# Kernel optimization log

Hardware: AMD Instinct MI355X
Metric: run time of the kernel (lower is better)

## Reference

```python
import jax, jax.numpy as jnp
import numpy as np

KS = 3            # kernel_size
DILS = (1, 2, 4)  # dilation_list == padding_list
EPS = 1e-5        # BN eps


def _unfold3(x, d):
    # emulate F.unfold(kernel=3, dilation=d, padding=d, stride=1).view(b, c, 9, h, w)
    b, c, h, w = x.shape
    xp = jnp.pad(x, ((0, 0), (0, 0), (d, d), (d, d)))
    pats = [xp[:, :, i * d:i * d + h, j * d:j * d + w] for i in range(KS) for j in range(KS)]
    return jnp.stack(pats, axis=2)


def _conv1x1(x, w, b):
    return jnp.einsum('bchw,oc->bohw', x, w) + b[None, :, None, None]


def _bn_relu(x, g, be, m, v):
    s = g / jnp.sqrt(v + EPS)
    return jax.nn.relu(x * s[None, :, None, None] + (be - m * s)[None, :, None, None])


def _proj(x, w1, b1, g1, be1, m1, v1, w2, b2, g2, be2, m2, v2):
    h = _bn_relu(_conv1x1(x, w1, b1), g1, be1, m1, v1)
    return _bn_relu(_conv1x1(h, w2, b2), g2, be2, m2, v2)


def setup_inputs():
    key = jax.random.key(0)
    Cin, Ck, Cv, Cout = 512, 256, 256, 512
    B, H, W = 4, 64, 64
    ks = iter(jax.random.split(key, 48))

    def nrm(shape, s=0.02):
        return jax.random.normal(next(ks), shape, jnp.float32) * s

    def bn(c):
        return (jnp.ones((c,), jnp.float32) + nrm((c,), 0.1),  # gamma
                nrm((c,), 0.1),                                 # beta
                nrm((c,), 0.1),                                 # running mean
                jax.random.uniform(next(ks), (c,), jnp.float32, 0.5, 1.5))  # running var

    inp = {"x": jax.random.normal(next(ks), (B, Cin, H, W), jnp.float32)}
    for p in ("k", "q"):
        g1, be1, m1, v1 = bn(Ck)
        g2, be2, m2, v2 = bn(Ck)
        inp.update({
            p + "1_w": nrm((Ck, Cin)), p + "1_b": nrm((Ck,)),
            p + "1_g": g1, p + "1_be": be1, p + "1_m": m1, p + "1_v": v1,
            p + "2_w": nrm((Ck, Ck)), p + "2_b": nrm((Ck,)),
            p + "2_g": g2, p + "2_be": be2, p + "2_m": m2, p + "2_v": v2,
        })
    inp["v_w"] = nrm((Cv, Cin)); inp["v_b"] = nrm((Cv,))
    inp["w_w"] = nrm((Cout, Cv)); inp["w_b"] = nrm((Cout,))
    return inp


def reference(x,
              k1_w, k1_b, k1_g, k1_be, k1_m, k1_v,
              k2_w, k2_b, k2_g, k2_be, k2_m, k2_v,
              q1_w, q1_b, q1_g, q1_be, q1_m, q1_v,
              q2_w, q2_b, q2_g, q2_be, q2_m, q2_v,
              v_w, v_b, w_w, w_b):
    # scale == 1: MaxPool2d(1x1-equivalent) and final bilinear resize are identities.
    value = _conv1x1(x, v_w, v_b)                                  # (b,cv,h,w)
    keyf = _proj(x, k1_w, k1_b, k1_g, k1_be, k1_m, k1_v,
                 k2_w, k2_b, k2_g, k2_be, k2_m, k2_v)              # (b,ck,h,w)
    query = _proj(x, q1_w, q1_b, q1_g, q1_be, q1_m, q1_v,
                  q2_w, q2_b, q2_g, q2_be, q2_m, q2_v)             # (b,ck,h,w)
    uk = jnp.concatenate([_unfold3(keyf, d) for d in DILS], axis=2)   # (b,ck,27,h,w)
    uv = jnp.concatenate([_unfold3(value, d) for d in DILS], axis=2)  # (b,cv,27,h,w)
    sim = jnp.sum(uk * query[:, :, None], axis=1, keepdims=True)      # (b,1,27,h,w)
    sim = jax.nn.softmax(sim, axis=2)
    context = jnp.sum(sim * uv, axis=2)                               # (b,cv,h,w)
    return _conv1x1(context, w_w, w_b)
```

## Files before the change

### kernel.cpp

```cpp
#include <hip/hip_runtime.h>

#define HW   4096
#define Hh   64
#define Ww   64
#define NB   27
#define EPSBN 1e-5f

typedef _Float16 f16x8 __attribute__((ext_vector_type(8)));
typedef _Float16 f16x4 __attribute__((ext_vector_type(4)));
typedef _Float16 f16x2 __attribute__((ext_vector_type(2)));
typedef float    f32x4 __attribute__((ext_vector_type(4)));

__device__ __forceinline__ void gld_lds16(const void* g, void* l) {
    __builtin_amdgcn_global_load_lds(
        (const __attribute__((address_space(1))) unsigned int*)g,
        (__attribute__((address_space(3))) unsigned int*)l, 16, 0, 0);
}

__global__ __launch_bounds__(256)
void cvt_w_kernel(const float* s0, const float* s1, const float* s2,
                  const float* s3, const float* s4, const float* s5,
                  _Float16* d0, _Float16* d1, _Float16* d2,
                  _Float16* d3, _Float16* d4, _Float16* d5)
{
    const int j = blockIdx.y;
    const float* s = j==0?s0: j==1?s1: j==2?s2: j==3?s3: j==4?s4: s5;
    _Float16*  d = j==0?d0: j==1?d1: j==2?d2: j==3?d3: j==4?d4: d5;
    const int  n = (j==3 || j==4) ? 65536 : 131072;
    const int  i = (blockIdx.x * 256 + threadIdx.x) * 8;
    if (i < n) {
        f16x8 h;
        #pragma unroll
        for (int k = 0; k < 8; ++k) h[k] = (_Float16)s[i + k];
        *(f16x8*)(d + i) = h;
    }
}

__global__ __launch_bounds__(256)
void cvt_x_kernel(const float* __restrict__ x, _Float16* __restrict__ xT)
{
    const int tx = threadIdx.x;
    const int ty = threadIdx.y;
    const int p  = blockIdx.x * 64 + tx;
    const int c0 = blockIdx.y * 32 + ty * 8;
    const int b  = blockIdx.z;
    const float* xp = x + ((size_t)b * 512 + c0) * HW + p;
    f16x8 h;
    #pragma unroll
    for (int i = 0; i < 8; ++i) h[i] = (_Float16)xp[(size_t)i * HW];
    *(f16x8*)(xT + ((size_t)b * HW + p) * 512 + c0) = h;
}

struct GJob {
    const _Float16* in;
    const _Float16* w;
    const float* b; const float* g; const float* be; const float* m; const float* v;
    _Float16* oh;
    float*    of;
};

__global__ __launch_bounds__(256)
void gemm128(GJob J0, GJob J1, GJob J2, int nmb0, int nmb01,
             int K, int JO, int mode)
{
    __shared__ _Float16 As[128 * 64];
    __shared__ _Float16 Bs[128 * 64];

    const int tid  = threadIdx.x;
    const int lane = tid & 63;
    const int w    = tid >> 6;
    const int lr   = lane & 15;
    const int lg   = lane >> 4;
    const int wm   = w & 1;
    const int wn   = w >> 1;

    const int bx = blockIdx.x;
    const int nb = (bx & 7) * 16 + (bx >> 3);
    const int mb = blockIdx.y;

    const bool i0 = mb < nmb0;
    const bool i1 = !i0 && mb < nmb01;
#define SELJ(f) (i0 ? J0.f : (i1 ? J1.f : J2.f))
    const _Float16* Jin = SELJ(in);
    const _Float16* Jw  = SELJ(w);
    const float* Jb  = SELJ(b);
    const float* Jg  = SELJ(g);
    const float* Jbe = SELJ(be);
    const float* Jm  = SELJ(m);
    const float* Jv  = SELJ(v);
    _Float16* Joh = SELJ(oh);
    float*    Jof = SELJ(of);
#undef SELJ
    const int obase = (mb - (i0 ? 0 : (i1 ? nmb0 : nmb01))) * 128;

    const int rowS = w * 32 + (lane >> 3);
    const int scol = (((lane & 7) ^ (lane >> 3)) << 3);
    const _Float16* aSrc = Jw  + (size_t)(obase + rowS) * K + scol;
    const _Float16* bSrc = Jin + (size_t)(nb * 128 + rowS) * K + scol;
    char* aDst = (char*)As + w * 4096;
    char* bDst = (char*)Bs + w * 4096;

    f32x4 acc[4][4] = {};

    const int nr = K >> 6;
    for (int rd = 0; rd < nr; ++rd) {
        __syncthreads();
        const int kb = rd * 64;
        #pragma unroll
        for (int j = 0; j < 4; ++j)
            gld_lds16(aSrc + (size_t)j * 8 * K + kb, aDst + j * 1024);
        #pragma unroll
        for (int j = 0; j < 4; ++j)
            gld_lds16(bSrc + (size_t)j * 8 * K + kb, bDst + j * 1024);
        __syncthreads();

        #pragma unroll
        for (int ks = 0; ks < 2; ++ks) {
            const int colx = (ks * 64 + lg * 16) ^ ((lr & 7) << 4);
            f16x8 afr[4], bfr[4];
            #pragma unroll
            for (int t = 0; t < 4; ++t) {
                afr[t] = *(const f16x8*)((const char*)As + (wm * 64 + t * 16 + lr) * 128 + colx);
                bfr[t] = *(const f16x8*)((const char*)Bs + (wn * 64 + t * 16 + lr) * 128 + colx);
            }
            #pragma unroll
            for (int ai = 0; ai < 4; ++ai)
                #pragma unroll
                for (int bj = 0; bj < 4; ++bj)
                    acc[ai][bj] = __builtin_amdgcn_mfma_f32_16x16x32_f16(
                        afr[ai], bfr[bj], acc[ai][bj], 0, 0, 0);
        }
    }

    const int relu = (Jg != nullptr);
    #pragma unroll
    for (int ai = 0; ai < 4; ++ai) {
        const int o4 = obase + wm * 64 + ai * 16 + lg * 4;
        float sc[4], of_[4];
        #pragma unroll
        for (int r = 0; r < 4; ++r) {
            const int o = o4 + r;
            if (Jg) { float s = Jg[o] * rsqrtf(Jv[o] + EPSBN); sc[r] = s; of_[r] = fmaf(Jb[o] - Jm[o], s, Jbe[o]); }
            else    { sc[r] = 1.f; of_[r] = Jb[o]; }
        }
        #pragma unroll
        for (int bj = 0; bj < 4; ++bj) {
            const int pg = nb * 128 + wn * 64 + bj * 16 + lr;
            float vv[4];
            #pragma unroll
            for (int r = 0; r < 4; ++r) {
                float t = fmaf(acc[ai][bj][r], sc[r], of_[r]);
                vv[r] = relu ? fmaxf(t, 0.f) : t;
            }
            if (mode == 0) {
                f16x4 h;
                #pragma unroll
                for (int r = 0; r < 4; ++r) h[r] = (_Float16)vv[r];
                *(f16x4*)(Joh + (size_t)pg * JO + o4) = h;
            } else {
                #pragma unroll
                for (int r = 0; r < 4; ++r)
                    Jof[((size_t)(pg >> 12) * JO + o4 + r) * HW + (pg & 4095)] = vv[r];
            }
        }
    }
}

__global__ __launch_bounds__(256)
void attn_fused(const _Float16* __restrict__ keyT, const _Float16* __restrict__ qryT,
                const _Float16* __restrict__ valT, _Float16* __restrict__ ctxT)
{
    const int tid  = threadIdx.x;
    const int slot = tid & 31;
    const int b    = blockIdx.y;
    const int p    = blockIdx.x * 8 + (tid >> 5);
    const int y    = p >> 6;
    const int xc   = p & 63;

    int   idx[NB];
    float valf[NB];
    #pragma unroll
    for (int n = 0; n < NB; ++n) {
        const int d  = (n < 9) ? 1 : (n < 18 ? 2 : 4);
        const int i  = (n / 3) % 3 - 1;
        const int j  = n % 3 - 1;
        const int yy = y + i * d, xx = xc + j * d;
        const bool ok = ((unsigned)yy < (unsigned)Hh) && ((unsigned)xx < (unsigned)Ww);
        idx[n]  = min(max(yy, 0), Hh - 1) * Ww + min(max(xx, 0), Ww - 1);
        valf[n] = ok ? 1.f : 0.f;
    }

    const size_t base = (size_t)b * HW * 256 + slot * 8;
    const f16x8 q8 = *(const f16x8*)(qryT + base + (size_t)p * 256);

    f16x2 qp[4];
    #pragma unroll
    for (int i = 0; i < 4; ++i)
        qp[i] = __builtin_shufflevector(q8, q8, 0, 1);
    qp[0] = __builtin_shufflevector(q8, q8, 0, 1);
    qp[1] = __builtin_shufflevector(q8, q8, 2, 3);
    qp[2] = __builtin_shufflevector(q8, q8, 4, 5);
    qp[3] = __builtin_shufflevector(q8, q8, 6, 7);

    float sim[NB];
    #pragma unroll
    for (int n = 0; n < NB; ++n) {
        const f16x8 k8 = *(const f16x8*)(keyT + base + (size_t)idx[n] * 256);
        float s = 0.f;
        s = __builtin_amdgcn_fdot2(__builtin_shufflevector(k8, k8, 0, 1), qp[0], s, false);
        s = __builtin_amdgcn_fdot2(__builtin_shufflevector(k8, k8, 2, 3), qp[1], s, false);
        s = __builtin_amdgcn_fdot2(__builtin_shufflevector(k8, k8, 4, 5), qp[2], s, false);
        s = __builtin_amdgcn_fdot2(__builtin_shufflevector(k8, k8, 6, 7), qp[3], s, false);
        sim[n] = s;
    }

    #pragma unroll
    for (int n = 0; n < NB; ++n) {
        float s = sim[n];
        s += __shfl_xor(s, 1);
        s += __shfl_xor(s, 2);
        s += __shfl_xor(s, 4);
        s += __shfl_xor(s, 8);
        s += __shfl_xor(s, 16);
        sim[n] = s * valf[n];
    }

    float mx = sim[0];
    #pragma unroll
    for (int n = 1; n < NB; ++n) mx = fmaxf(mx, sim[n]);
    float sum = 0.f;
    #pragma unroll
    for (int n = 0; n < NB; ++n) { sim[n] = __expf(sim[n] - mx); sum += sim[n]; }
    const float inv = 1.f / sum;
    #pragma unroll
    for (int n = 0; n < NB; ++n) sim[n] = sim[n] * inv * valf[n];

    float acc[8];
    #pragma unroll
    for (int i = 0; i < 8; ++i) acc[i] = 0.f;
    #pragma unroll
    for (int n = 0; n < NB; ++n) {
        const f16x8 v8 = *(const f16x8*)(valT + base + (size_t)idx[n] * 256);
        const float w = sim[n];
        #pragma unroll
        for (int i = 0; i < 8; ++i) acc[i] = fmaf(w, (float)v8[i], acc[i]);
    }

    f16x8 h;
    #pragma unroll
    for (int i = 0; i < 8; ++i) h[i] = (_Float16)acc[i];
    *(f16x8*)(ctxT + base + (size_t)p * 256) = h;
}

extern "C" void kernel_launch(void* const* d_in, const int* in_sizes, int n_in,
                              void* d_out, int out_size, void* d_ws, size_t ws_size,
                              hipStream_t stream)
{
    (void)in_sizes; (void)n_in; (void)out_size; (void)ws_size;
    const float* x     = (const float*)d_in[0];
    const float* k1_w  = (const float*)d_in[1];
    const float* k1_b  = (const float*)d_in[2];
    const float* k1_g  = (const float*)d_in[3];
    const float* k1_be = (const float*)d_in[4];
    const float* k1_m  = (const float*)d_in[5];
    const float* k1_v  = (const float*)d_in[6];
    const float* k2_w  = (const float*)d_in[7];
    const float* k2_b  = (const float*)d_in[8];
    const float* k2_g  = (const float*)d_in[9];
    const float* k2_be = (const float*)d_in[10];
    const float* k2_m  = (const float*)d_in[11];
    const float* k2_v  = (const float*)d_in[12];
    const float* q1_w  = (const float*)d_in[13];
    const float* q1_b  = (const float*)d_in[14];
    const float* q1_g  = (const float*)d_in[15];
    const float* q1_be = (const float*)d_in[16];
    const float* q1_m  = (const float*)d_in[17];
    const float* q1_v  = (const float*)d_in[18];
    const float* q2_w  = (const float*)d_in[19];
    const float* q2_b  = (const float*)d_in[20];
    const float* q2_g  = (const float*)d_in[21];
    const float* q2_be = (const float*)d_in[22];
    const float* q2_m  = (const float*)d_in[23];
    const float* q2_v  = (const float*)d_in[24];
    const float* v_w   = (const float*)d_in[25];
    const float* v_b   = (const float*)d_in[26];
    const float* w_w   = (const float*)d_in[27];
    const float* w_b   = (const float*)d_in[28];

    _Float16* hw = (_Float16*)d_ws;
    const size_t SX = (size_t)4 * HW * 512;
    const size_t SH = (size_t)4 * HW * 256;
    _Float16* xT    = hw;
    _Float16* wv_h  = xT + SX;
    _Float16* wk1_h = wv_h  + 131072;
    _Float16* wq1_h = wk1_h + 131072;
    _Float16* wk2_h = wq1_h + 131072;
    _Float16* wq2_h = wk2_h + 65536;
    _Float16* ww_h  = wq2_h + 65536;
    _Float16* k1T   = ww_h  + 131072;
    _Float16* q1T   = k1T + SH;
    _Float16* valT  = q1T + SH;
    _Float16* ctxT  = valT + SH;
    _Float16* keyPC = ctxT + SH;
    _Float16* qryPC = keyPC + SH;

    cvt_w_kernel<<<dim3(64, 6), 256, 0, stream>>>(v_w, k1_w, q1_w, k2_w, q2_w, w_w,
                                                  wv_h, wk1_h, wq1_h, wk2_h, wq2_h, ww_h);
    cvt_x_kernel<<<dim3(64, 16, 4), dim3(64, 4), 0, stream>>>(x, xT);

    GJob jv  = { xT,  wv_h,  v_b,  nullptr, nullptr, nullptr, nullptr, valT,  nullptr };
    GJob jk1 = { xT,  wk1_h, k1_b, k1_g, k1_be, k1_m, k1_v,            k1T,   nullptr };
    GJob jq1 = { xT,  wq1_h, q1_b, q1_g, q1_be, q1_m, q1_v,            q1T,   nullptr };
    GJob jk2 = { k1T, wk2_h, k2_b, k2_g, k2_be, k2_m, k2_v,            keyPC, nullptr };
    GJob jq2 = { q1T, wq2_h, q2_b, q2_g, q2_be, q2_m, q2_v,            qryPC, nullptr };
    GJob jw  = { ctxT, ww_h, w_b,  nullptr, nullptr, nullptr, nullptr, nullptr, (float*)d_out };

    gemm128<<<dim3(128, 6), 256, 0, stream>>>(jv, jk1, jq1, 2, 4, 512, 256, 0);
    gemm128<<<dim3(128, 4), 256, 0, stream>>>(jk2, jq2, jq2, 2, 4, 256, 256, 0);
    attn_fused<<<dim3(512, 4), 256, 0, stream>>>(keyPC, qryPC, valT, ctxT);
    gemm128<<<dim3(128, 4), 256, 0, stream>>>(jw, jw, jw, 4, 4, 256, 512, 2);
}
```

Baseline: 96.65 us.

## Double-buffer GEMM LDS tiles and merge weight/input conversion into one LDS-transposed kernel

The GEMM now uses two LDS buffers per operand and issues global-to-LDS loads for the next K-slab before computing the current one, leaving one barrier per iteration instead of two. The weight cast and the x transpose kernels are merged into a single launch, and the x transpose is staged through a padded LDS tile so each block writes whole 1 KB rows of xT. This cuts a launch and aims to hide load latency in the GEMMs, but doubles GEMM LDS use (64 KB per block), which may lower occupancy. A redundant shuffle loop in the attention kernel is also removed.

```diff
diff --git a/kernel.cpp b/kernel.cpp
--- a/kernel.cpp
+++ b/kernel.cpp
@@ -18,37 +18,53 @@
 }
 
 __global__ __launch_bounds__(256)
-void cvt_w_kernel(const float* s0, const float* s1, const float* s2,
-                  const float* s3, const float* s4, const float* s5,
-                  _Float16* d0, _Float16* d1, _Float16* d2,
-                  _Float16* d3, _Float16* d4, _Float16* d5)
+void prep_kernel(const float* s0, const float* s1, const float* s2,
+                 const float* s3, const float* s4, const float* s5,
+                 _Float16* d0, _Float16* d1, _Float16* d2,
+                 _Float16* d3, _Float16* d4, _Float16* d5,
+                 const float* __restrict__ x, _Float16* __restrict__ xT)
 {
-    const int j = blockIdx.y;
-    const float* s = j==0?s0: j==1?s1: j==2?s2: j==3?s3: j==4?s4: s5;
-    _Float16*  d = j==0?d0: j==1?d1: j==2?d2: j==3?d3: j==4?d4: d5;
-    const int  n = (j==3 || j==4) ? 65536 : 131072;
-    const int  i = (blockIdx.x * 256 + threadIdx.x) * 8;
-    if (i < n) {
+    __shared__ _Float16 T[64][516];
+    const int bid = blockIdx.x;
+    const int tid = threadIdx.x;
+
+    if (bid < 384) {
+        const int j  = bid >> 6;
+        const int bx = bid & 63;
+        const float* s = j==0?s0: j==1?s1: j==2?s2: j==3?s3: j==4?s4: s5;
+        _Float16*  d = j==0?d0: j==1?d1: j==2?d2: j==3?d3: j==4?d4: d5;
+        const int  n = (j==3 || j==4) ? 65536 : 131072;
+        const int  i = (bx * 256 + tid) * 8;
+        if (i < n) {
+            f16x8 h;
+            #pragma unroll
+            for (int k = 0; k < 8; ++k) h[k] = (_Float16)s[i + k];
+            *(f16x8*)(d + i) = h;
+        }
+        return;
+    }
+    const int t  = bid - 384;
+    const int p0 = (t & 63) * 64;
+    const int b  = t >> 6;
+    const int tx = tid & 63;
+    const int ty = tid >> 6;
+
+    #pragma unroll 2
+    for (int ch = 0; ch < 16; ++ch) {
+        const int c0 = ch * 32 + ty * 8;
+        const float* xp = x + ((size_t)b * 512 + c0) * HW + p0 + tx;
         f16x8 h;
         #pragma unroll
-        for (int k = 0; k < 8; ++k) h[k] = (_Float16)s[i + k];
-        *(f16x8*)(d + i) = h;
-    }
-}
-
-__global__ __launch_bounds__(256)
-void cvt_x_kernel(const float* __restrict__ x, _Float16* __restrict__ xT)
-{
-    const int tx = threadIdx.x;
-    const int ty = threadIdx.y;
-    const int p  = blockIdx.x * 64 + tx;
-    const int c0 = blockIdx.y * 32 + ty * 8;
-    const int b  = blockIdx.z;
-    const float* xp = x + ((size_t)b * 512 + c0) * HW + p;
-    f16x8 h;
-    #pragma unroll
-    for (int i = 0; i < 8; ++i) h[i] = (_Float16)xp[(size_t)i * HW];
-    *(f16x8*)(xT + ((size_t)b * HW + p) * 512 + c0) = h;
+        for (int i = 0; i < 8; ++i) h[i] = (_Float16)xp[(size_t)i * HW];
+        *(f16x8*)&T[tx][c0] = h;
+    }
+    __syncthreads();
+    #pragma unroll 4
+    for (int rr = 0; rr < 16; ++rr) {
+        const int row = rr * 4 + ty;
+        f16x8 h = *(const f16x8*)&T[row][tx * 8];
+        *(f16x8*)(xT + ((size_t)b * HW + p0 + row) * 512 + tx * 8) = h;
+    }
 }
 
 struct GJob {
@@ -63,8 +79,8 @@
 void gemm128(GJob J0, GJob J1, GJob J2, int nmb0, int nmb01,
              int K, int JO, int mode)
 {
-    __shared__ _Float16 As[128 * 64];
-    __shared__ _Float16 Bs[128 * 64];
+    __shared__ _Float16 As[2][128 * 64];
+    __shared__ _Float16 Bs[2][128 * 64];
 
     const int tid  = threadIdx.x;
     const int lane = tid & 63;
@@ -97,31 +113,36 @@
     const int scol = (((lane & 7) ^ (lane >> 3)) << 3);
     const _Float16* aSrc = Jw  + (size_t)(obase + rowS) * K + scol;
     const _Float16* bSrc = Jin + (size_t)(nb * 128 + rowS) * K + scol;
-    char* aDst = (char*)As + w * 4096;
-    char* bDst = (char*)Bs + w * 4096;
+
+    auto STAGE = [&](int buf, int rd) {
+        const int kb = rd * 64;
+        char* aD = (char*)&As[buf][0] + w * 4096;
+        char* bD = (char*)&Bs[buf][0] + w * 4096;
+        #pragma unroll
+        for (int j = 0; j < 4; ++j)
+            gld_lds16(aSrc + (size_t)j * 8 * K + kb, aD + j * 1024);
+        #pragma unroll
+        for (int j = 0; j < 4; ++j)
+            gld_lds16(bSrc + (size_t)j * 8 * K + kb, bD + j * 1024);
+    };
 
     f32x4 acc[4][4] = {};
 
     const int nr = K >> 6;
+    STAGE(0, 0);
+    __syncthreads();
+
+    int cur = 0;
     for (int rd = 0; rd < nr; ++rd) {
-        __syncthreads();
-        const int kb = rd * 64;
-        #pragma unroll
-        for (int j = 0; j < 4; ++j)
-            gld_lds16(aSrc + (size_t)j * 8 * K + kb, aDst + j * 1024);
-        #pragma unroll
-        for (int j = 0; j < 4; ++j)
-            gld_lds16(bSrc + (size_t)j * 8 * K + kb, bDst + j * 1024);
-        __syncthreads();
-
+        if (rd + 1 < nr) STAGE(cur ^ 1, rd + 1);
         #pragma unroll
         for (int ks = 0; ks < 2; ++ks) {
             const int colx = (ks * 64 + lg * 16) ^ ((lr & 7) << 4);
             f16x8 afr[4], bfr[4];
             #pragma unroll
             for (int t = 0; t < 4; ++t) {
-                afr[t] = *(const f16x8*)((const char*)As + (wm * 64 + t * 16 + lr) * 128 + colx);
-                bfr[t] = *(const f16x8*)((const char*)Bs + (wn * 64 + t * 16 + lr) * 128 + colx);
+                afr[t] = *(const f16x8*)((const char*)&As[cur][0] + (wm * 64 + t * 16 + lr) * 128 + colx);
+                bfr[t] = *(const f16x8*)((const char*)&Bs[cur][0] + (wn * 64 + t * 16 + lr) * 128 + colx);
             }
             #pragma unroll
             for (int ai = 0; ai < 4; ++ai)
@@ -130,6 +151,8 @@
                     acc[ai][bj] = __builtin_amdgcn_mfma_f32_16x16x32_f16(
                         afr[ai], bfr[bj], acc[ai][bj], 0, 0, 0);
         }
+        __syncthreads();
+        cur ^= 1;
     }
 
     const int relu = (Jg != nullptr);
@@ -194,9 +217,6 @@
     const f16x8 q8 = *(const f16x8*)(qryT + base + (size_t)p * 256);
 
     f16x2 qp[4];
-    #pragma unroll
-    for (int i = 0; i < 4; ++i)
-        qp[i] = __builtin_shufflevector(q8, q8, 0, 1);
     qp[0] = __builtin_shufflevector(q8, q8, 0, 1);
     qp[1] = __builtin_shufflevector(q8, q8, 2, 3);
     qp[2] = __builtin_shufflevector(q8, q8, 4, 5);
@@ -304,9 +324,9 @@
     _Float16* keyPC = ctxT + SH;
     _Float16* qryPC = keyPC + SH;
 
-    cvt_w_kernel<<<dim3(64, 6), 256, 0, stream>>>(v_w, k1_w, q1_w, k2_w, q2_w, w_w,
-                                                  wv_h, wk1_h, wq1_h, wk2_h, wq2_h, ww_h);
-    cvt_x_kernel<<<dim3(64, 16, 4), dim3(64, 4), 0, stream>>>(x, xT);
+    prep_kernel<<<640, 256, 0, stream>>>(v_w, k1_w, q1_w, k2_w, q2_w, w_w,
+                                         wv_h, wk1_h, wq1_h, wk2_h, wq2_h, ww_h,
+                                         x, xT);
 
     GJob jv  = { xT,  wv_h,  v_b,  nullptr, nullptr, nullptr, nullptr, valT,  nullptr };
     GJob jk1 = { xT,  wk1_h, k1_b, k1_g, k1_be, k1_m, k1_v,            k1T,   nullptr };
```

After: 98.35 us. No clear change (+1.8%).
